# Optimization experiments

Measured on AMD Instinct MI355X. Metric: run time of the kernel, lower is better.

The kernel has to match this reference:

```python
import jax, jax.numpy as jnp
import numpy as np

HIDDEN = 512
OUTDIM = 256
D = (HIDDEN + 1) * (HIDDEN + 1)
EPS = 1e-5


def setup_inputs() -> dict:
    key = jax.random.key(0)
    k1, k2, k3, k4 = jax.random.split(key, 4)
    B = 128
    a = jax.random.normal(k1, (B, HIDDEN), dtype=jnp.float32)
    v = jax.random.normal(k2, (B, HIDDEN), dtype=jnp.float32)
    # learned params
    ln_gamma = jnp.ones((D,), dtype=jnp.float32)
    ln_beta = jnp.zeros((D,), dtype=jnp.float32)
    W = jax.random.normal(k3, (OUTDIM, D), dtype=jnp.float32) / np.sqrt(D)
    b = jax.random.normal(k4, (OUTDIM,), dtype=jnp.float32) * 0.01
    return {"a": a, "v": v, "ln_gamma": ln_gamma, "ln_beta": ln_beta, "W": W, "b": b}


def reference(a, v, ln_gamma, ln_beta, W, b):
    B = a.shape[0]
    ones = jnp.ones((B, 1), dtype=a.dtype)
    ah = jnp.concatenate([ones, a], axis=1)  # [B, H+1]
    vh = jnp.concatenate([ones, v], axis=1)  # [B, H+1]
    # rank-1 outer product, flattened: [B, (H+1)^2]
    fusion = jnp.einsum('bi,bj->bij', ah, vh).reshape(B, D)
    # LayerNorm over last dim
    mu = jnp.mean(fusion, axis=-1, keepdims=True)
    var = jnp.mean(jnp.square(fusion - mu), axis=-1, keepdims=True)
    normed = (fusion - mu) / jnp.sqrt(var + EPS) * ln_gamma + ln_beta
    # dropout = identity (eval mode)
    out = jax.nn.relu(normed @ W.T + b)
    return out
```

## Files before the change

### kernel.cpp

```cpp
#include <hip/hip_runtime.h>
#include <hip/hip_bf16.h>

#define HID 512
#define OD  256
#define HP  513
#define EPSV 1e-5f

typedef float f32x16 __attribute__((ext_vector_type(16)));
typedef short s16x8  __attribute__((ext_vector_type(8)));

static __device__ __forceinline__ unsigned short f2bf(float f) {
    union { float f; unsigned u; } x; x.f = f;
    unsigned r = x.u + 0x7FFFu + ((x.u >> 16) & 1u);
    return (unsigned short)(r >> 16);
}
static __device__ __forceinline__ unsigned pkbf(float x, float y) {
    float2 t; t.x = x; t.y = y;
    __hip_bfloat162 h = __float22bfloat162_rn(t);
    union { __hip_bfloat162 h; unsigned u; } c; c.h = h;
    return c.u;
}
static __device__ __forceinline__ float bfu(unsigned short u) {
    union { unsigned q; float f; } cv; cv.q = ((unsigned)u) << 16;
    return cv.f;
}


__global__ void prep_all(const float* __restrict__ a, const float* __restrict__ v,
                         const float* __restrict__ gamma, const float* __restrict__ beta,
                         unsigned short* __restrict__ gpb, unsigned short* __restrict__ bpb,
                         unsigned short* __restrict__ vhT, float* __restrict__ vh512,
                         float* __restrict__ ahT) {
    int b = blockIdx.x, t = threadIdx.x;
    if (b < HP) {
        int ii = b;
        for (int s = t; s < 512; s += 256) {
            int half = s >> 8, ss = s & 255, ll = ss >> 3, c = ss & 7;
            int j = half * 256 + c * 32 + ll;
            gpb[(size_t)ii * 512 + s] = f2bf(gamma[(size_t)ii * HP + j]);
            bpb[(size_t)ii * 512 + s] = f2bf(beta [(size_t)ii * HP + j]);
        }
    } else if (b < HP + 128) {
        int m = b - HP;
        for (int s = t; s < 512; s += 256) {
            int half = s >> 8, ss = s & 255, ll = ss >> 3, c = ss & 7;
            int j = half * 256 + c * 32 + ll;
            float val = (j == 0) ? 1.f : v[m * HID + j - 1];
            vhT[(size_t)m * 512 + s] = f2bf(val);
        }
    } else if (b == HP + 128) {
        if (t < 128) vh512[t] = v[t * HID + 511];
    } else {
        int idx = (b - HP - 129) * 256 + t;
        if (idx < HP * 128) {
            int i = idx >> 7, m = idx & 127;
            ahT[idx] = (i == 0) ? 1.f : a[m * HID + i - 1];
        }
    }
}

__global__ void prep_w5(const float* __restrict__ W, const float* __restrict__ gamma,
                        const float* __restrict__ beta,
                        float* __restrict__ w5g, float* __restrict__ w5b) {
    int oi = blockIdx.x * 256 + threadIdx.x;
    if (oi < OD * HP) {
        unsigned ii = (unsigned)oi % 513u;
        float wv = W[(size_t)oi * 513u + 512u];
        w5g[oi] = gamma[(size_t)ii * HP + 512] * wv;
        w5b[oi] = beta [(size_t)ii * HP + 512] * wv;
    }
}

__global__ void stats_kernel(const float* __restrict__ a, const float* __restrict__ v,
                             float* __restrict__ mu, float* __restrict__ rsig) {
    __shared__ float s1[256], s2[256], s3[256], s4[256];
    int m = blockIdx.x, t = threadIdx.x;
    float a0 = a[m * HID + t], a1 = a[m * HID + t + 256];
    float v0 = v[m * HID + t], v1 = v[m * HID + t + 256];
    s1[t] = a0 + a1; s2[t] = a0 * a0 + a1 * a1;
    s3[t] = v0 + v1; s4[t] = v0 * v0 + v1 * v1;
    __syncthreads();
    for (int off = 128; off > 0; off >>= 1) {
        if (t < off) { s1[t] += s1[t + off]; s2[t] += s2[t + off];
                       s3[t] += s3[t + off]; s4[t] += s4[t + off]; }
        __syncthreads();
    }
    if (t == 0) {
        float Sa = 1.f + s1[0], Qa = 1.f + s2[0];
        float Sv = 1.f + s3[0], Qv = 1.f + s4[0];
        float muv = Sa * Sv / (float)((float)HP * (float)HP);
        float var = Qa * Qv / (float)((float)HP * (float)HP) - muv * muv;
        mu[m]   = muv;
        rsig[m] = rsqrtf(var + EPSV);
    }
}

__global__ __launch_bounds__(512, 2) void stage_fused(
        const float* __restrict__ W, const unsigned short* __restrict__ gpb,
        const unsigned short* __restrict__ bpb, const unsigned short* __restrict__ vhT,
        const float* __restrict__ ahT,
        float* __restrict__ Pout, float* __restrict__ Sgo, float* __restrict__ Sbo) {
    __shared__ __align__(16) char Bs[131072];
    __shared__ __align__(16) char bt[2][16384];

    const int tid = threadIdx.x, lane = tid & 63, w = tid >> 6;
    const int l31 = lane & 31, kg = lane >> 5;
    const int cr = 2 * w + kg;
    const int colm = (w & 3) * 32 + l31;
    const int kslb = (w >> 2) * 8;
    const int o = blockIdx.x;
    const unsigned rbase = (unsigned)o * 513u;

#pragma unroll
    for (int q0 = 0; q0 < 16; q0 += 4) {
        uint4 vals[4];
#pragma unroll
        for (int qq = 0; qq < 4; ++qq) {
            int idx = tid + (q0 + qq) * 512;
            int mr = idx >> 6, c = idx & 63;
            vals[qq] = *(const uint4*)(vhT + (size_t)mr * 512 + c * 8);
        }
#pragma unroll
        for (int qq = 0; qq < 4; ++qq) {
            int idx = tid + (q0 + qq) * 512;
            int mr = idx >> 6, c = idx & 63;
            *(uint4*)(&Bs[mr * 1024 + ((c * 16) ^ ((mr & 15) << 4))]) = vals[qq];
        }
    }

    float WrA[16], WrB[16];
    uint4 gaA1, gaA2, gaB1, gaB2;
    float ahv[16];
    f32x16 acc;
#pragma unroll
    for (int e = 0; e < 16; ++e) acc[e] = 0.f;
    float psum = 0.f, sg = 0.f, sb = 0.f;

    auto LOADW = [&](int g, int half, float (&dst)[16]) {
        const float* p1 = W + (size_t)(rbase + (unsigned)(g * 32 + cr)) * 513u + half * 256 + l31;
        const float* p2 = p1 + 16 * 513;
#pragma unroll
        for (int c = 0; c < 8; ++c) { dst[c] = p1[c * 32]; dst[8 + c] = p2[c * 32]; }
    };
    auto LOADG = [&](int g, int half, uint4& u1, uint4& u2) {
        u1 = *(const uint4*)(gpb + ((size_t)(g * 32 + cr) << 9) + half * 256 + l31 * 8);
        u2 = *(const uint4*)(gpb + ((size_t)(g * 32 + cr + 16) << 9) + half * 256 + l31 * 8);
    };
    auto CONVROW = [&](const float* Wc, const uint4 gc, const uint4 b4, int row, char* tile) {
        const unsigned gw[4] = {gc.x, gc.y, gc.z, gc.w};
        const unsigned bw[4] = {b4.x, b4.y, b4.z, b4.w};
        float p[8];
        float s = 0.f, t2 = 0.f;
#pragma unroll
        for (int e = 0; e < 8; ++e) {
            unsigned ug = (e & 1) ? (gw[e >> 1] >> 16) : (gw[e >> 1] & 0xffffu);
            unsigned ub = (e & 1) ? (bw[e >> 1] >> 16) : (bw[e >> 1] & 0xffffu);
            p[e] = bfu((unsigned short)ug) * Wc[e];
            s += p[e];
            t2 = fmaf(bfu((unsigned short)ub), Wc[e], t2);
        }
        uint4 o4;
        o4.x = pkbf(p[0], p[1]); o4.y = pkbf(p[2], p[3]);
        o4.z = pkbf(p[4], p[5]); o4.w = pkbf(p[6], p[7]);
        *(uint4*)(tile + row * 512 + ((l31 * 16) ^ ((row & 15) << 4))) = o4;
        sg += s; sb += t2;
    };

    LOADW(0, 0, WrA); LOADG(0, 0, gaA1, gaA2);
    __syncthreads();

#pragma unroll 1
    for (int g = 0; g < 16; ++g) {
        uint4 bb1 = *(const uint4*)(bpb + ((size_t)(g * 32 + cr) << 9) + l31 * 8);
        uint4 bb2 = *(const uint4*)(bpb + ((size_t)(g * 32 + cr + 16) << 9) + l31 * 8);
        LOADW(g, 1, WrB); LOADG(g, 1, gaB1, gaB2);
        CONVROW(&WrA[0], gaA1, bb1, cr,      bt[0]);
        CONVROW(&WrA[8], gaA2, bb2, cr + 16, bt[0]);

        __builtin_amdgcn_sched_barrier(0);
        asm volatile("s_waitcnt lgkmcnt(0)" ::: "memory");
        __builtin_amdgcn_s_barrier();
        __builtin_amdgcn_sched_barrier(0);

#pragma unroll
        for (int i2 = 0; i2 < 8; ++i2) {
            int ksl = kslb + i2;
            s16x8 afr = *(const s16x8*)(&bt[0][l31 * 512 +
                          ((ksl * 32 + kg * 16) ^ ((l31 & 15) << 4))]);
            s16x8 bfr = *(const s16x8*)(&Bs[colm * 1024 +
                          ((ksl * 32 + kg * 16) ^ ((colm & 15) << 4))]);
            acc = __builtin_amdgcn_mfma_f32_32x32x16_bf16(afr, bfr, acc, 0, 0, 0);
        }

        uint4 cb1 = *(const uint4*)(bpb + ((size_t)(g * 32 + cr) << 9) + 256 + l31 * 8);
        uint4 cb2 = *(const uint4*)(bpb + ((size_t)(g * 32 + cr + 16) << 9) + 256 + l31 * 8);
        if (g < 15) { LOADW(g + 1, 0, WrA); LOADG(g + 1, 0, gaA1, gaA2); }
#pragma unroll
        for (int e = 0; e < 16; ++e) {
            int row32 = (e & 3) + 8 * (e >> 2) + 4 * kg;
            ahv[e] = ahT[(size_t)(g * 32 + row32) * 128 + colm];
        }
        CONVROW(&WrB[0], gaB1, cb1, cr,      bt[1]);
        CONVROW(&WrB[8], gaB2, cb2, cr + 16, bt[1]);

        __builtin_amdgcn_sched_barrier(0);
        asm volatile("s_waitcnt lgkmcnt(0)" ::: "memory");
        __builtin_amdgcn_s_barrier();
        __builtin_amdgcn_sched_barrier(0);

#pragma unroll
        for (int i2 = 0; i2 < 8; ++i2) {
            int ksl = kslb + i2;
            s16x8 afr = *(const s16x8*)(&bt[1][l31 * 512 +
                          ((ksl * 32 + kg * 16) ^ ((l31 & 15) << 4))]);
            s16x8 bfr = *(const s16x8*)(&Bs[colm * 1024 +
                          ((512 + ksl * 32 + kg * 16) ^ ((colm & 15) << 4))]);
            acc = __builtin_amdgcn_mfma_f32_32x32x16_bf16(afr, bfr, acc, 0, 0, 0);
        }
#pragma unroll
        for (int e = 0; e < 16; ++e) psum = fmaf(acc[e], ahv[e], psum);
#pragma unroll
        for (int e = 0; e < 16; ++e) acc[e] = 0.f;
    }

    __syncthreads();
    float* redP  = (float*)Bs;
    float* redSg = redP + 256;
    float* redSb = redP + 264;
    psum += __shfl_xor(psum, 32);
#pragma unroll
    for (int off = 1; off < 64; off <<= 1) {
        sg += __shfl_xor(sg, off); sb += __shfl_xor(sb, off);
    }
    if (lane < 32) redP[colm * 2 + (w >> 2)] = psum;
    if (lane == 0) { redSg[w] = sg; redSb[w] = sb; }
    __syncthreads();
    if (tid < 128) Pout[(size_t)o * 128 + tid] = redP[tid * 2] + redP[tid * 2 + 1];
    if (tid == 0) {
        float S = 0.f, T = 0.f;
#pragma unroll
        for (int k = 0; k < 8; ++k) { S += redSg[k]; T += redSb[k]; }
        Sgo[o] = S; Sbo[o] = T;
    }
}

__global__ void finalize_kernel(const float* __restrict__ Pout, const float* __restrict__ Sgo,
                                const float* __restrict__ Sbo, const float* __restrict__ w5g,
                                const float* __restrict__ w5b, const float* __restrict__ ahT,
                                const float* __restrict__ vh512, const unsigned short* __restrict__ vhT,
                                const float* __restrict__ W, const float* __restrict__ gamma,
                                const float* __restrict__ beta, const float* __restrict__ mu,
                                const float* __restrict__ rsig, const float* __restrict__ bias,
                                float* __restrict__ out) {
    __shared__ float wg[HP], wb[HP], gws[512], bws[512];
    int o = blockIdx.x, m = threadIdx.x;
    for (int i = m; i < HP; i += 128) {
        wg[i] = w5g[(size_t)o * HP + i];
        wb[i] = w5b[(size_t)o * HP + i];
    }
    for (int j = m; j < 512; j += 128) {
        float wv = W[((size_t)o * 513u + 512u) * 513u + j];
        int s = ((j >> 8) << 8) + ((j & 31) << 3) + ((j & 255) >> 5);
        gws[s] = gamma[(size_t)512 * HP + j] * wv;
        bws[s] = beta [(size_t)512 * HP + j] * wv;
    }
    __syncthreads();
    float Pf = 0.f, Sgf = 0.f, Sbf = 0.f;
    for (int i = 0; i < HP; ++i) {
        float g = wg[i];
        Pf = fmaf(ahT[(size_t)i * 128 + m], g, Pf);
        Sgf += g; Sbf += wb[i];
    }
    float dot = 0.f, Sg2 = 0.f, Sb2 = 0.f;
    const unsigned short* vr = vhT + (size_t)m * 512;
    for (int s = 0; s < 512; ++s) {
        float g = gws[s];
        dot = fmaf(bfu(vr[s]), g, dot);
        Sg2 += g; Sb2 += bws[s];
    }
    float P  = Pout[(size_t)o * 128 + m] + vh512[m] * Pf + ahT[(size_t)512 * 128 + m] * dot;
    float Sg = Sgo[o] + Sgf + Sg2;
    float Sb = Sbo[o] + Sbf + Sb2;
    float x = rsig[m] * (P - mu[m] * Sg) + Sb + bias[o];
    out[m * OD + o] = fmaxf(x, 0.f);
}

extern "C" void kernel_launch(void* const* d_in, const int* in_sizes, int n_in,
                              void* d_out, int out_size, void* d_ws, size_t ws_size,
                              hipStream_t stream) {
    const float* a     = (const float*)d_in[0];
    const float* v     = (const float*)d_in[1];
    const float* gamma = (const float*)d_in[2];
    const float* beta  = (const float*)d_in[3];
    const float* W     = (const float*)d_in[4];
    const float* bias  = (const float*)d_in[5];
    float* out = (float*)d_out;

    float* cur = (float*)d_ws;
    float* mu    = cur; cur += 128;
    float* rsig  = cur; cur += 128;
    float* Sgo   = cur; cur += 256;
    float* Sbo   = cur; cur += 256;
    float* Pout  = cur; cur += (size_t)OD * 128;
    float* ahT   = cur; cur += (size_t)HP * 128;
    float* vh512 = cur; cur += 128;
    float* w5g   = cur; cur += (size_t)OD * HP;
    float* w5b   = cur; cur += (size_t)OD * HP;
    unsigned short* gpb = (unsigned short*)cur;
    unsigned short* bpb = gpb + (size_t)HP * 512;
    unsigned short* vhT = bpb + (size_t)HP * 512;

    prep_all<<<HP + 128 + 1 + 257, 256, 0, stream>>>(a, v, gamma, beta, gpb, bpb, vhT, vh512, ahT);
    prep_w5<<<HP, 256, 0, stream>>>(W, gamma, beta, w5g, w5b);
    stats_kernel<<<128, 256, 0, stream>>>(a, v, mu, rsig);
    stage_fused<<<OD, 512, 0, stream>>>(W, gpb, bpb, vhT, ahT, Pout, Sgo, Sbo);
    finalize_kernel<<<OD, 128, 0, stream>>>(Pout, Sgo, Sbo, w5g, w5b, ahT, vh512, vhT,
                                            W, gamma, beta, mu, rsig, bias, out);
}
```

Before: 105.8 us.

## Merge prep kernels, reschedule stage prefetch, and split finalize across two halves

Folds the stats kernel into prep_all as extra blocks, and drops prep_w5 by computing the W column-512 products directly inside finalize. The main fused kernel now prefetches the next group's W, gamma and beta halves one phase earlier, so global loads overlap the MFMA work. Finalize uses 256 threads and splits each reduction into two halves combined through shared memory. This removes two launches and the w5 workspace traffic, at the cost of more register pressure from the extra prefetch buffers and strided W reads moved into finalize.

```diff
diff --git a/kernel.cpp b/kernel.cpp
--- a/kernel.cpp
+++ b/kernel.cpp
@@ -30,7 +30,9 @@
                          const float* __restrict__ gamma, const float* __restrict__ beta,
                          unsigned short* __restrict__ gpb, unsigned short* __restrict__ bpb,
                          unsigned short* __restrict__ vhT, float* __restrict__ vh512,
-                         float* __restrict__ ahT) {
+                         float* __restrict__ ahT, float* __restrict__ mu,
+                         float* __restrict__ rsig) {
+    __shared__ float s1[256], s2[256], s3[256], s4[256];
     int b = blockIdx.x, t = threadIdx.x;
     if (b < HP) {
         int ii = b;
@@ -50,48 +52,32 @@
         }
     } else if (b == HP + 128) {
         if (t < 128) vh512[t] = v[t * HID + 511];
-    } else {
+    } else if (b < HP + 129 + 257) {
         int idx = (b - HP - 129) * 256 + t;
         if (idx < HP * 128) {
             int i = idx >> 7, m = idx & 127;
             ahT[idx] = (i == 0) ? 1.f : a[m * HID + i - 1];
         }
-    }
-}
-
-__global__ void prep_w5(const float* __restrict__ W, const float* __restrict__ gamma,
-                        const float* __restrict__ beta,
-                        float* __restrict__ w5g, float* __restrict__ w5b) {
-    int oi = blockIdx.x * 256 + threadIdx.x;
-    if (oi < OD * HP) {
-        unsigned ii = (unsigned)oi % 513u;
-        float wv = W[(size_t)oi * 513u + 512u];
-        w5g[oi] = gamma[(size_t)ii * HP + 512] * wv;
-        w5b[oi] = beta [(size_t)ii * HP + 512] * wv;
-    }
-}
-
-__global__ void stats_kernel(const float* __restrict__ a, const float* __restrict__ v,
-                             float* __restrict__ mu, float* __restrict__ rsig) {
-    __shared__ float s1[256], s2[256], s3[256], s4[256];
-    int m = blockIdx.x, t = threadIdx.x;
-    float a0 = a[m * HID + t], a1 = a[m * HID + t + 256];
-    float v0 = v[m * HID + t], v1 = v[m * HID + t + 256];
-    s1[t] = a0 + a1; s2[t] = a0 * a0 + a1 * a1;
-    s3[t] = v0 + v1; s4[t] = v0 * v0 + v1 * v1;
-    __syncthreads();
-    for (int off = 128; off > 0; off >>= 1) {
-        if (t < off) { s1[t] += s1[t + off]; s2[t] += s2[t + off];
-                       s3[t] += s3[t + off]; s4[t] += s4[t + off]; }
+    } else {
+        int m = b - (HP + 129 + 257);
+        float a0 = a[m * HID + t], a1 = a[m * HID + t + 256];
+        float v0 = v[m * HID + t], v1 = v[m * HID + t + 256];
+        s1[t] = a0 + a1; s2[t] = a0 * a0 + a1 * a1;
+        s3[t] = v0 + v1; s4[t] = v0 * v0 + v1 * v1;
         __syncthreads();
-    }
-    if (t == 0) {
-        float Sa = 1.f + s1[0], Qa = 1.f + s2[0];
-        float Sv = 1.f + s3[0], Qv = 1.f + s4[0];
-        float muv = Sa * Sv / (float)((float)HP * (float)HP);
-        float var = Qa * Qv / (float)((float)HP * (float)HP) - muv * muv;
-        mu[m]   = muv;
-        rsig[m] = rsqrtf(var + EPSV);
+        for (int off = 128; off > 0; off >>= 1) {
+            if (t < off) { s1[t] += s1[t + off]; s2[t] += s2[t + off];
+                           s3[t] += s3[t + off]; s4[t] += s4[t + off]; }
+            __syncthreads();
+        }
+        if (t == 0) {
+            float Sa = 1.f + s1[0], Qa = 1.f + s2[0];
+            float Sv = 1.f + s3[0], Qv = 1.f + s4[0];
+            float muv = Sa * Sv / (float)((float)HP * (float)HP);
+            float var = Qa * Qv / (float)((float)HP * (float)HP) - muv * muv;
+            mu[m]   = muv;
+            rsig[m] = rsqrtf(var + EPSV);
+        }
     }
 }
 
@@ -130,6 +116,7 @@
 
     float WrA[16], WrB[16];
     uint4 gaA1, gaA2, gaB1, gaB2;
+    uint4 bbA1, bbA2, bbB1, bbB2;
     float ahv[16];
     f32x16 acc;
 #pragma unroll
@@ -146,6 +133,10 @@
         u1 = *(const uint4*)(gpb + ((size_t)(g * 32 + cr) << 9) + half * 256 + l31 * 8);
         u2 = *(const uint4*)(gpb + ((size_t)(g * 32 + cr + 16) << 9) + half * 256 + l31 * 8);
     };
+    auto LOADB = [&](int g, int half, uint4& u1, uint4& u2) {
+        u1 = *(const uint4*)(bpb + ((size_t)(g * 32 + cr) << 9) + half * 256 + l31 * 8);
+        u2 = *(const uint4*)(bpb + ((size_t)(g * 32 + cr + 16) << 9) + half * 256 + l31 * 8);
+    };
     auto CONVROW = [&](const float* Wc, const uint4 gc, const uint4 b4, int row, char* tile) {
         const unsigned gw[4] = {gc.x, gc.y, gc.z, gc.w};
         const unsigned bw[4] = {b4.x, b4.y, b4.z, b4.w};
@@ -167,15 +158,21 @@
     };
 
     LOADW(0, 0, WrA); LOADG(0, 0, gaA1, gaA2);
+    LOADW(0, 1, WrB); LOADG(0, 1, gaB1, gaB2);
+    LOADB(0, 0, bbA1, bbA2);
     __syncthreads();
 
 #pragma unroll 1
     for (int g = 0; g < 16; ++g) {
-        uint4 bb1 = *(const uint4*)(bpb + ((size_t)(g * 32 + cr) << 9) + l31 * 8);
-        uint4 bb2 = *(const uint4*)(bpb + ((size_t)(g * 32 + cr + 16) << 9) + l31 * 8);
-        LOADW(g, 1, WrB); LOADG(g, 1, gaB1, gaB2);
-        CONVROW(&WrA[0], gaA1, bb1, cr,      bt[0]);
-        CONVROW(&WrA[8], gaA2, bb2, cr + 16, bt[0]);
+        CONVROW(&WrA[0], gaA1, bbA1, cr,      bt[0]);
+        CONVROW(&WrA[8], gaA2, bbA2, cr + 16, bt[0]);
+        if (g < 15) { LOADW(g + 1, 0, WrA); LOADG(g + 1, 0, gaA1, gaA2); }
+        LOADB(g, 1, bbB1, bbB2);
+#pragma unroll
+        for (int e = 0; e < 16; ++e) {
+            int row32 = (e & 3) + 8 * (e >> 2) + 4 * kg;
+            ahv[e] = ahT[(size_t)(g * 32 + row32) * 128 + colm];
+        }
 
         __builtin_amdgcn_sched_barrier(0);
         asm volatile("s_waitcnt lgkmcnt(0)" ::: "memory");
@@ -192,16 +189,12 @@
             acc = __builtin_amdgcn_mfma_f32_32x32x16_bf16(afr, bfr, acc, 0, 0, 0);
         }
 
-        uint4 cb1 = *(const uint4*)(bpb + ((size_t)(g * 32 + cr) << 9) + 256 + l31 * 8);
-        uint4 cb2 = *(const uint4*)(bpb + ((size_t)(g * 32 + cr + 16) << 9) + 256 + l31 * 8);
-        if (g < 15) { LOADW(g + 1, 0, WrA); LOADG(g + 1, 0, gaA1, gaA2); }
-#pragma unroll
-        for (int e = 0; e < 16; ++e) {
-            int row32 = (e & 3) + 8 * (e >> 2) + 4 * kg;
-            ahv[e] = ahT[(size_t)(g * 32 + row32) * 128 + colm];
-        }
-        CONVROW(&WrB[0], gaB1, cb1, cr,      bt[1]);
-        CONVROW(&WrB[8], gaB2, cb2, cr + 16, bt[1]);
+        CONVROW(&WrB[0], gaB1, bbB1, cr,      bt[1]);
+        CONVROW(&WrB[8], gaB2, bbB2, cr + 16, bt[1]);
+        if (g < 15) {
+            LOADW(g + 1, 1, WrB); LOADG(g + 1, 1, gaB1, gaB2);
+            LOADB(g + 1, 0, bbA1, bbA2);
+        }
 
         __builtin_amdgcn_sched_barrier(0);
         asm volatile("s_waitcnt lgkmcnt(0)" ::: "memory");
@@ -245,44 +238,55 @@
 }
 
 __global__ void finalize_kernel(const float* __restrict__ Pout, const float* __restrict__ Sgo,
-                                const float* __restrict__ Sbo, const float* __restrict__ w5g,
-                                const float* __restrict__ w5b, const float* __restrict__ ahT,
+                                const float* __restrict__ Sbo, const float* __restrict__ ahT,
                                 const float* __restrict__ vh512, const unsigned short* __restrict__ vhT,
                                 const float* __restrict__ W, const float* __restrict__ gamma,
                                 const float* __restrict__ beta, const float* __restrict__ mu,
                                 const float* __restrict__ rsig, const float* __restrict__ bias,
                                 float* __restrict__ out) {
     __shared__ float wg[HP], wb[HP], gws[512], bws[512];
-    int o = blockIdx.x, m = threadIdx.x;
-    for (int i = m; i < HP; i += 128) {
-        wg[i] = w5g[(size_t)o * HP + i];
-        wb[i] = w5b[(size_t)o * HP + i];
-    }
-    for (int j = m; j < 512; j += 128) {
-        float wv = W[((size_t)o * 513u + 512u) * 513u + j];
+    __shared__ float redP[2][128], redD[2][128], redS[4];
+    int o = blockIdx.x, tid = threadIdx.x;
+    int m = tid & 127, h = tid >> 7;
+    for (int i = tid; i < HP; i += 256) {
+        float wv = W[((size_t)((unsigned)o * 513u + (unsigned)i)) * 513u + 512u];
+        wg[i] = gamma[(size_t)i * HP + 512] * wv;
+        wb[i] = beta [(size_t)i * HP + 512] * wv;
+    }
+    for (int j = tid; j < 512; j += 256) {
+        float wv = W[((size_t)((unsigned)o * 513u + 512u)) * 513u + j];
         int s = ((j >> 8) << 8) + ((j & 31) << 3) + ((j & 255) >> 5);
         gws[s] = gamma[(size_t)512 * HP + j] * wv;
         bws[s] = beta [(size_t)512 * HP + j] * wv;
     }
     __syncthreads();
+    int i0 = h ? 257 : 0, i1 = h ? 513 : 257;
     float Pf = 0.f, Sgf = 0.f, Sbf = 0.f;
-    for (int i = 0; i < HP; ++i) {
+    for (int i = i0; i < i1; ++i) {
         float g = wg[i];
         Pf = fmaf(ahT[(size_t)i * 128 + m], g, Pf);
         Sgf += g; Sbf += wb[i];
     }
-    float dot = 0.f, Sg2 = 0.f, Sb2 = 0.f;
+    int s0 = h * 256, s1 = s0 + 256;
+    float dot = 0.f;
     const unsigned short* vr = vhT + (size_t)m * 512;
-    for (int s = 0; s < 512; ++s) {
+    for (int s = s0; s < s1; ++s) {
         float g = gws[s];
         dot = fmaf(bfu(vr[s]), g, dot);
-        Sg2 += g; Sb2 += bws[s];
-    }
-    float P  = Pout[(size_t)o * 128 + m] + vh512[m] * Pf + ahT[(size_t)512 * 128 + m] * dot;
-    float Sg = Sgo[o] + Sgf + Sg2;
-    float Sb = Sbo[o] + Sbf + Sb2;
-    float x = rsig[m] * (P - mu[m] * Sg) + Sb + bias[o];
-    out[m * OD + o] = fmaxf(x, 0.f);
+        Sgf += g; Sbf += bws[s];
+    }
+    redP[h][m] = Pf; redD[h][m] = dot;
+    if (m == 0) { redS[h * 2] = Sgf; redS[h * 2 + 1] = Sbf; }
+    __syncthreads();
+    if (h == 0) {
+        float P = Pout[(size_t)o * 128 + m]
+                + vh512[m] * (redP[0][m] + redP[1][m])
+                + ahT[(size_t)512 * 128 + m] * (redD[0][m] + redD[1][m]);
+        float Sg = Sgo[o] + redS[0] + redS[2];
+        float Sb = Sbo[o] + redS[1] + redS[3];
+        float x = rsig[m] * (P - mu[m] * Sg) + Sb + bias[o];
+        out[m * OD + o] = fmaxf(x, 0.f);
+    }
 }
 
 extern "C" void kernel_launch(void* const* d_in, const int* in_sizes, int n_in,
@@ -304,16 +308,13 @@
     float* Pout  = cur; cur += (size_t)OD * 128;
     float* ahT   = cur; cur += (size_t)HP * 128;
     float* vh512 = cur; cur += 128;
-    float* w5g   = cur; cur += (size_t)OD * HP;
-    float* w5b   = cur; cur += (size_t)OD * HP;
     unsigned short* gpb = (unsigned short*)cur;
     unsigned short* bpb = gpb + (size_t)HP * 512;
     unsigned short* vhT = bpb + (size_t)HP * 512;
 
-    prep_all<<<HP + 128 + 1 + 257, 256, 0, stream>>>(a, v, gamma, beta, gpb, bpb, vhT, vh512, ahT);
-    prep_w5<<<HP, 256, 0, stream>>>(W, gamma, beta, w5g, w5b);
-    stats_kernel<<<128, 256, 0, stream>>>(a, v, mu, rsig);
+    prep_all<<<HP + 129 + 257 + 128, 256, 0, stream>>>(a, v, gamma, beta, gpb, bpb,
+                                                       vhT, vh512, ahT, mu, rsig);
     stage_fused<<<OD, 512, 0, stream>>>(W, gpb, bpb, vhT, ahT, Pout, Sgo, Sbo);
-    finalize_kernel<<<OD, 128, 0, stream>>>(Pout, Sgo, Sbo, w5g, w5b, ahT, vh512, vhT,
+    finalize_kernel<<<OD, 256, 0, stream>>>(Pout, Sgo, Sbo, ahT, vh512, vhT,
                                             W, gamma, beta, mu, rsig, bias, out);
 }
```

After: 148.4 us. +40.3%, slower.
